# Kernel optimization log

Hardware: AMD Instinct MI355X
Metric: run time of the kernel (lower is better)

## Reference

```python
import jax, jax.numpy as jnp
import numpy as np

TEMPERATURE = 0.5
EPS = 1e-8  # torch CosineSimilarity default eps


def setup_inputs() -> dict:
    key = jax.random.key(0)
    k1, k2 = jax.random.split(key)
    B, D = 4096, 256
    z_i = jax.random.normal(k1, (B, D), dtype=jnp.float32)
    z_j = jax.random.normal(k2, (B, D), dtype=jnp.float32)
    return {"z_i": z_i, "z_j": z_j}


def _normalize(x):
    # torch cosine_similarity clamps each norm at eps
    n = jnp.maximum(jnp.linalg.norm(x, axis=-1, keepdims=True), EPS)
    return x / n


def reference(z_i, z_j):
    B = z_i.shape[0]
    z = jnp.concatenate([z_i, z_j], axis=0)            # [2B, D]
    zn = _normalize(z)                                  # [2B, D]
    sim = jnp.einsum('id,jd->ij', zn, zn) / TEMPERATURE  # [2B, 2B]
    sim_exp = jnp.exp(sim)
    mask = jnp.eye(2 * B, dtype=bool)
    sim_sum = jnp.sum(jnp.where(mask, 0.0, sim_exp), axis=1)  # [2B]
    # positive pair similarity, computed on original (unconcatenated) pairs
    zi_n = _normalize(z_i)
    zj_n = _normalize(z_j)
    pos = jnp.exp(jnp.sum(zi_n * zj_n, axis=-1) / TEMPERATURE)  # [B]
    pos = jnp.concatenate([pos, pos], axis=0)          # [2B]
    loss = -jnp.log(pos / sim_sum)
    return jnp.mean(loss)
```

## Files before the change

### kernel.cpp

```cpp
#include <hip/hip_runtime.h>
#include <hip/hip_bf16.h>
#include <stdint.h>


#define BROWS 4096
#define DIM   256
#define N2    8192

typedef __attribute__((ext_vector_type(4))) float          f32x4;
typedef __attribute__((ext_vector_type(8))) short          s16x8;
typedef __attribute__((ext_vector_type(4))) unsigned short u16x4;

#define S_EXP  1.6986436597467051f
#define LN2    0.6931471805599453f

__device__ inline unsigned short f2bf(float f) {
    uint32_t b = __float_as_uint(f);
    b += 0x7fffu + ((b >> 16) & 1u);
    return (unsigned short)(b >> 16);
}
__device__ inline float bf2f(unsigned short u) {
    return __uint_as_float(((uint32_t)u) << 16);
}

__device__ inline void gload_lds16(const void* g, void* l) {
    __builtin_amdgcn_global_load_lds(
        (const __attribute__((address_space(1))) uint32_t*)g,
        (__attribute__((address_space(3))) uint32_t*)l, 16, 0, 0);
}

__device__ inline float wave_reduce(float v) {
    #pragma unroll
    for (int m = 1; m < 64; m <<= 1) v += __shfl_xor(v, m);
    return v;
}

__global__ __launch_bounds__(256) void k_norm_pos(const float* __restrict__ zi,
                                                  const float* __restrict__ zj,
                                                  unsigned short* __restrict__ zn,
                                                  float* __restrict__ diag,
                                                  float* __restrict__ posv,
                                                  unsigned int* __restrict__ counter) {
    if (blockIdx.x == 0 && threadIdx.x == 0) *counter = 0u;
    int i    = blockIdx.x * 4 + (threadIdx.x >> 6);
    int lane = threadIdx.x & 63;
    f32x4 a = *(const f32x4*)(zi + (size_t)i * DIM + lane * 4);
    f32x4 b = *(const f32x4*)(zj + (size_t)i * DIM + lane * 4);
    float ssa = a[0]*a[0] + a[1]*a[1] + a[2]*a[2] + a[3]*a[3];
    float ssb = b[0]*b[0] + b[1]*b[1] + b[2]*b[2] + b[3]*b[3];
    float dab = a[0]*b[0] + a[1]*b[1] + a[2]*b[2] + a[3]*b[3];
    ssa = wave_reduce(ssa);
    ssb = wave_reduce(ssb);
    dab = wave_reduce(dab);
    float na = 1.0f / fmaxf(sqrtf(ssa), 1e-8f);
    float nb = 1.0f / fmaxf(sqrtf(ssb), 1e-8f);
    if (lane == 0) posv[i] = 2.0f * dab * na * nb;

    float sa = na * S_EXP, sb = nb * S_EXP;
    u16x4 oa, ob;
    float da = 0.0f, db = 0.0f;
    #pragma unroll
    for (int k = 0; k < 4; ++k) {
        unsigned short ua = f2bf(a[k] * sa);
        unsigned short ub = f2bf(b[k] * sb);
        oa[k] = ua; ob[k] = ub;
        float fa = bf2f(ua), fb = bf2f(ub);
        da += fa * fa; db += fb * fb;
    }
    *(u16x4*)(zn + (size_t)i * DIM + lane * 4)           = oa;
    *(u16x4*)(zn + (size_t)(i + BROWS) * DIM + lane * 4) = ob;
    da = wave_reduce(da);
    db = wave_reduce(db);
    if (lane == 0) { diag[i] = da; diag[i + BROWS] = db; }
}

__global__ __launch_bounds__(256, 2) void k_simsum(const unsigned short* __restrict__ zn,
                                                   float* __restrict__ partial) {
    __shared__ unsigned short lds[2][64 * DIM];
    int bid = blockIdx.x;
    int rb = bid & 63;
    int cc = bid >> 6;
    int rowbase = rb * 128;
    int colbase = cc * 1024;
    int tid = threadIdx.x, lane = tid & 63, w = tid >> 6;
    int cl = lane & 15, g = lane >> 4;

    s16x8 afrag[2][8];
    #pragma unroll
    for (int rt = 0; rt < 2; ++rt) {
        int row = rowbase + w * 32 + rt * 16 + cl;
        const unsigned short* ap = zn + (size_t)row * DIM + g * 8;
        #pragma unroll
        for (int kc = 0; kc < 8; ++kc)
            afrag[rt][kc] = *(const s16x8*)(ap + kc * 32);
    }

    float pp[2][4];
    #pragma unroll
    for (int rt = 0; rt < 2; ++rt)
        #pragma unroll
        for (int r = 0; r < 4; ++r) pp[rt][r] = 0.0f;

    auto stage = [&](int buf, int s) {
        int crow = colbase + s * 64 + lane;
        const unsigned short* gsrc = zn + (size_t)crow * DIM;
        char* base = (char*)&lds[buf][0];
        #pragma unroll
        for (int i = 0; i < 8; ++i)
            gload_lds16(gsrc + i * 32 + w * 8, base + i * 4096 + w * 1024);
    };

    stage(0, 0);
    __syncthreads();

    for (int s = 0; s < 16; ++s) {
        int cur = s & 1;
        if (s < 15) stage(cur ^ 1, s + 1);

        const char* lbase = (const char*)&lds[cur][0];
        #pragma unroll
        for (int ct = 0; ct < 4; ++ct) {
            f32x4 acc[2];
            acc[0] = (f32x4){0.f, 0.f, 0.f, 0.f};
            acc[1] = (f32x4){0.f, 0.f, 0.f, 0.f};
            #pragma unroll
            for (int kc = 0; kc < 8; ++kc) {
                s16x8 bfrag = *(const s16x8*)(lbase + kc * 4096 + g * 1024 +
                                              (ct * 16 + cl) * 16);
                acc[0] = __builtin_amdgcn_mfma_f32_16x16x32_bf16(afrag[0][kc], bfrag, acc[0], 0, 0, 0);
                acc[1] = __builtin_amdgcn_mfma_f32_16x16x32_bf16(afrag[1][kc], bfrag, acc[1], 0, 0, 0);
            }
            #pragma unroll
            for (int rt = 0; rt < 2; ++rt)
                #pragma unroll
                for (int r = 0; r < 4; ++r)
                    pp[rt][r] += __builtin_amdgcn_exp2f(acc[rt][r]);
        }
        __syncthreads();
    }

    #pragma unroll
    for (int rt = 0; rt < 2; ++rt) {
        #pragma unroll
        for (int r = 0; r < 4; ++r) {
            float v = pp[rt][r];
            v += __shfl_xor(v, 1);
            v += __shfl_xor(v, 2);
            v += __shfl_xor(v, 4);
            v += __shfl_xor(v, 8);
            if (cl == 0)
                partial[(size_t)cc * N2 + rowbase + w * 32 + rt * 16 + g * 4 + r] = v;
        }
    }
}

__global__ __launch_bounds__(256) void k_loss(const float* __restrict__ partial,
                                              const float* __restrict__ diag,
                                              const float* __restrict__ posv,
                                              float* __restrict__ blocksum,
                                              unsigned int* __restrict__ counter,
                                              float* __restrict__ out) {
    int row = blockIdx.x * 256 + threadIdx.x;
    float sum = 0.0f;
    #pragma unroll
    for (int c = 0; c < 8; ++c) sum += partial[(size_t)c * N2 + row];
    sum -= __builtin_amdgcn_exp2f(diag[row]);
    float lr = __builtin_amdgcn_logf(sum) * LN2 - posv[row & (BROWS - 1)];
    lr = wave_reduce(lr);
    __shared__ float red[4];
    if ((threadIdx.x & 63) == 0) red[threadIdx.x >> 6] = lr;
    __syncthreads();
    if (threadIdx.x == 0) {
        blocksum[blockIdx.x] = red[0] + red[1] + red[2] + red[3];
        __threadfence();
        unsigned int old = atomicAdd(counter, 1u);
        if (old == 31u) {
            __threadfence();
            volatile const float* bs = blocksum;
            float t = 0.0f;
            for (int i = 0; i < 32; ++i) t += bs[i];
            out[0] = t * (1.0f / N2);
        }
    }
}

extern "C" void kernel_launch(void* const* d_in, const int* in_sizes, int n_in,
                              void* d_out, int out_size, void* d_ws, size_t ws_size,
                              hipStream_t stream) {
    const float* zi = (const float*)d_in[0];
    const float* zj = (const float*)d_in[1];
    float* out = (float*)d_out;

    char* ws = (char*)d_ws;
    unsigned short* zn    = (unsigned short*)ws;
    float* diag           = (float*)(ws + (4u << 20));
    float* posv           = (float*)(ws + (4u << 20) + (32u << 10));
    float* blocksum       = (float*)(ws + (4u << 20) + (48u << 10));
    unsigned int* counter = (unsigned int*)(ws + (4u << 20) + (52u << 10));
    float* partial        = (float*)(ws + (4u << 20) + (64u << 10));

    k_norm_pos<<<BROWS / 4, 256, 0, stream>>>(zi, zj, zn, diag, posv, counter);
    k_simsum<<<512, 256, 0, stream>>>(zn, partial);
    k_loss<<<32, 256, 0, stream>>>(partial, diag, posv, blocksum, counter, out);
}
```

Baseline: 54.48 us.

## Triple-buffer column tiles with raw waitcnt barriers and MFMA priority boosts

Replaces the two 64-row LDS buffers with three 32-row buffers and keeps two stages of global-to-LDS loads in flight. Each step synchronizes with a hand-written s_waitcnt vmcnt plus s_barrier instead of __syncthreads, so the barrier waits only for the older stage. It also raises wave priority around the MFMA chain. The aim is to hide load latency and cut barrier stalls. The cost is twice as many barriers per column and reliance on exact vmcnt accounting for correctness.

```diff
diff --git a/kernel.cpp b/kernel.cpp
--- a/kernel.cpp
+++ b/kernel.cpp
@@ -76,7 +76,10 @@
 
 __global__ __launch_bounds__(256, 2) void k_simsum(const unsigned short* __restrict__ zn,
                                                    float* __restrict__ partial) {
-    __shared__ unsigned short lds[2][64 * DIM];
+    __shared__ unsigned short buf0[32 * DIM];
+    __shared__ unsigned short buf1[32 * DIM];
+    __shared__ unsigned short buf2[32 * DIM];
+
     int bid = blockIdx.x;
     int rb = bid & 63;
     int cc = bid >> 6;
@@ -101,43 +104,57 @@
         #pragma unroll
         for (int r = 0; r < 4; ++r) pp[rt][r] = 0.0f;
 
-    auto stage = [&](int buf, int s) {
-        int crow = colbase + s * 64 + lane;
-        const unsigned short* gsrc = zn + (size_t)crow * DIM;
-        char* base = (char*)&lds[buf][0];
-        #pragma unroll
-        for (int i = 0; i < 8; ++i)
-            gload_lds16(gsrc + i * 32 + w * 8, base + i * 4096 + w * 1024);
+    auto stage_into = [&](char* bufbase, int s) {
+        const unsigned short* p = zn + (size_t)(colbase + s * 32 + (lane & 31)) * DIM
+                                  + (lane >> 5) * 8;
+        char* d = bufbase + (2 * w) * 2048;
+        gload_lds16(p + (2 * w) * 32,          d);
+        gload_lds16(p + (2 * w) * 32 + 8,      d + 1024);
+        gload_lds16(p + (2 * w + 1) * 32,      d + 2048);
+        gload_lds16(p + (2 * w + 1) * 32 + 8,  d + 3072);
     };
 
-    stage(0, 0);
-    __syncthreads();
-
-    for (int s = 0; s < 16; ++s) {
-        int cur = s & 1;
-        if (s < 15) stage(cur ^ 1, s + 1);
-
-        const char* lbase = (const char*)&lds[cur][0];
-        #pragma unroll
-        for (int ct = 0; ct < 4; ++ct) {
-            f32x4 acc[2];
-            acc[0] = (f32x4){0.f, 0.f, 0.f, 0.f};
-            acc[1] = (f32x4){0.f, 0.f, 0.f, 0.f};
-            #pragma unroll
-            for (int kc = 0; kc < 8; ++kc) {
-                s16x8 bfrag = *(const s16x8*)(lbase + kc * 4096 + g * 1024 +
-                                              (ct * 16 + cl) * 16);
-                acc[0] = __builtin_amdgcn_mfma_f32_16x16x32_bf16(afrag[0][kc], bfrag, acc[0], 0, 0, 0);
-                acc[1] = __builtin_amdgcn_mfma_f32_16x16x32_bf16(afrag[1][kc], bfrag, acc[1], 0, 0, 0);
-            }
-            #pragma unroll
-            for (int rt = 0; rt < 2; ++rt)
-                #pragma unroll
-                for (int r = 0; r < 4; ++r)
-                    pp[rt][r] += __builtin_amdgcn_exp2f(acc[rt][r]);
+    #define STEP(BUFR, BUFW, SIDX, DO_STAGE, WAITSTR)                              \
+        {                                                                          \
+            if (DO_STAGE) stage_into((char*)BUFW, (SIDX) + 2);                     \
+            const char* lbase_ = (const char*)BUFR;                               \
+            _Pragma("unroll")                                                      \
+            for (int ct = 0; ct < 2; ++ct) {                                       \
+                f32x4 acc0 = (f32x4){0.f,0.f,0.f,0.f};                             \
+                f32x4 acc1 = (f32x4){0.f,0.f,0.f,0.f};                             \
+                __builtin_amdgcn_s_setprio(1);                                     \
+                _Pragma("unroll")                                                  \
+                for (int kc = 0; kc < 8; ++kc) {                                   \
+                    s16x8 bfrag = *(const s16x8*)(lbase_ + kc * 2048 + g * 512 +   \
+                                                  (ct * 16 + cl) * 16);            \
+                    acc0 = __builtin_amdgcn_mfma_f32_16x16x32_bf16(                \
+                               afrag[0][kc], bfrag, acc0, 0, 0, 0);                \
+                    acc1 = __builtin_amdgcn_mfma_f32_16x16x32_bf16(                \
+                               afrag[1][kc], bfrag, acc1, 0, 0, 0);                \
+                }                                                                  \
+                __builtin_amdgcn_s_setprio(0);                                     \
+                _Pragma("unroll")                                                  \
+                for (int r = 0; r < 4; ++r) {                                      \
+                    pp[0][r] += __builtin_amdgcn_exp2f(acc0[r]);                   \
+                    pp[1][r] += __builtin_amdgcn_exp2f(acc1[r]);                   \
+                }                                                                  \
+            }                                                                      \
+            asm volatile(WAITSTR ::: "memory");                                    \
         }
-        __syncthreads();
-    }
+
+    stage_into((char*)buf0, 0);
+    stage_into((char*)buf1, 1);
+    asm volatile("s_waitcnt vmcnt(4)\ns_barrier" ::: "memory");
+
+    #pragma unroll 1
+    for (int s3 = 0; s3 < 30; s3 += 3) {
+        STEP(buf0, buf2, s3,     true, "s_waitcnt vmcnt(4)\ns_barrier")
+        STEP(buf1, buf0, s3 + 1, true, "s_waitcnt vmcnt(4)\ns_barrier")
+        STEP(buf2, buf1, s3 + 2, true, "s_waitcnt vmcnt(4)\ns_barrier")
+    }
+    STEP(buf0, buf2, 30, false, "s_waitcnt vmcnt(0)\ns_barrier")
+    STEP(buf1, buf0, 31, false, "")
+    #undef STEP
 
     #pragma unroll
     for (int rt = 0; rt < 2; ++rt) {
```

After: 59.28 us. 1.09x slower.
